# Kernel tuning notes

Hardware: AMD Instinct MI355X
Metric: run time of the kernel (lower is better)

Reference implementation:

```python
import jax, jax.numpy as jnp
import numpy as np

B, NI, NO = 32, 64, 64


def setup_inputs() -> dict:
    key = jax.random.key(0)
    k1, k2, k3, k4, k5, k6 = jax.random.split(key, 6)
    return {
        "input_re": jax.random.normal(k1, (B, NI, NI), dtype=jnp.float32),
        "input_im": jax.random.normal(k2, (B, NI, NI), dtype=jnp.float32),
        "w_re": jax.random.normal(k3, (NI, NI, NO, NO), dtype=jnp.float32),
        "w_im": jax.random.normal(k4, (NI, NI, NO, NO), dtype=jnp.float32),
        "amp_weights": jax.random.normal(k5, (NI, NI), dtype=jnp.float32),
        "phase_weights": jax.random.normal(k6, (NI, NI), dtype=jnp.float32),
    }


def reference(input_re, input_im, w_re, w_im, amp_weights, phase_weights):
    # complex input field (B, NI, NI) and diffraction kernel (NI, NI, NO, NO)
    e_in = jax.lax.complex(input_re, input_im)
    w_ip = jax.lax.complex(w_re, w_im)
    # passive transmission coefficients: sigmoid(amp) * exp(i*phase)
    ts = (jax.nn.sigmoid(amp_weights)
          * jnp.exp(1j * phase_weights.astype(jnp.complex64))).astype(jnp.complex64)
    # modulated field, then sum over input pixels (i,j) -> complex GEMM
    modulated = e_in * ts[None, :, :]                    # (B, NI, NI)
    out = jnp.einsum('bij,ijkl->bkl', modulated, w_ip)   # (B, NO, NO)
    return out
```

## Files before the change

kernel.cpp:

```cpp
#include <hip/hip_runtime.h>
#include <cstdint>
#include <cstddef>

#define KC 4096
#define NN 4096
#define NB 32
#define HALF (NB * NN)

typedef __attribute__((ext_vector_type(8))) short  bf16x8;
typedef __attribute__((ext_vector_type(16))) float f32x16;

__device__ __forceinline__ unsigned short f2bf(float f) {
    union { float f; unsigned u; } v; v.f = f;
    unsigned r = v.u + 0x7fffu + ((v.u >> 16) & 1u);
    return (unsigned short)(r >> 16);
}

__global__ __launch_bounds__(256) void prep_kernel(
    const float* __restrict__ in_re, const float* __restrict__ in_im,
    const float* __restrict__ amp,   const float* __restrict__ phase,
    uint32_t* __restrict__ wsA)
{
    int tid = blockIdx.x * 256 + threadIdx.x;
    int b = tid >> 12;
    int k = tid & (KC - 1);
    float er = in_re[tid], ei = in_im[tid];
    float a = amp[k], p = phase[k];
    float s = 1.0f / (1.0f + expf(-a));
    float sn, cs;
    sincosf(p, &sn, &cs);
    float tr = s * cs, ti = s * sn;
    float mr = er * tr - ei * ti;
    float mi = er * ti + ei * tr;
    uint32_t pk = (uint32_t)f2bf(mr) | ((uint32_t)f2bf(mi) << 16);
    wsA[((((k >> 2) << 5) + b) << 2) | (k & 3)] = pk;
}

__global__ __launch_bounds__(256) void gemm_kernel(
    const float* __restrict__ w_re, const float* __restrict__ w_im,
    const bf16x8* __restrict__ wsA, float2* __restrict__ wsP, int steps)
{
    const int lane = threadIdx.x & 63;
    const int wave = threadIdx.x >> 6;
    const int h    = lane >> 5;
    const int l32  = lane & 31;
    const int n    = blockIdx.x * 128 + wave * 32 + l32;
    const int s    = blockIdx.y;
    const int kbase = s * (steps * 8);

    f32x16 accR = {};
    f32x16 accI = {};

    const bf16x8* aptr = wsA + ((size_t)(kbase >> 2) + h) * 32 + l32;
    const float* pre = w_re + (size_t)(kbase + h * 4) * NN + n;
    const float* pim = w_im + (size_t)(kbase + h * 4) * NN + n;

#pragma unroll 4
    for (int t = 0; t < steps; ++t) {
        bf16x8 afrag = aptr[(size_t)(2 * t) * 32];
        const float* pr = pre + (size_t)t * 8 * NN;
        const float* pi = pim + (size_t)t * 8 * NN;
        float r0 = pr[0], r1 = pr[NN], r2 = pr[2 * NN], r3 = pr[3 * NN];
        float i0 = pi[0], i1 = pi[NN], i2 = pi[2 * NN], i3 = pi[3 * NN];

        bf16x8 bR, bI;
        bR[0] = (short)f2bf(r0);  bR[1] = (short)f2bf(-i0);
        bR[2] = (short)f2bf(r1);  bR[3] = (short)f2bf(-i1);
        bR[4] = (short)f2bf(r2);  bR[5] = (short)f2bf(-i2);
        bR[6] = (short)f2bf(r3);  bR[7] = (short)f2bf(-i3);
        bI[0] = (short)f2bf(i0);  bI[1] = (short)f2bf(r0);
        bI[2] = (short)f2bf(i1);  bI[3] = (short)f2bf(r1);
        bI[4] = (short)f2bf(i2);  bI[5] = (short)f2bf(r2);
        bI[6] = (short)f2bf(i3);  bI[7] = (short)f2bf(r3);

        accR = __builtin_amdgcn_mfma_f32_32x32x16_bf16(afrag, bR, accR, 0, 0, 0);
        accI = __builtin_amdgcn_mfma_f32_32x32x16_bf16(afrag, bI, accI, 0, 0, 0);
    }

#pragma unroll
    for (int r = 0; r < 16; ++r) {
        int brow = (r & 3) + 8 * (r >> 2) + 4 * h;
        float2 v; v.x = accR[r]; v.y = accI[r];
        wsP[((size_t)s * NB + brow) * NN + n] = v;
    }
}

__global__ __launch_bounds__(256) void reduce_kernel(
    const float2* __restrict__ wsP, float* __restrict__ out, int S)
{
    int tid = blockIdx.x * 256 + threadIdx.x;
    float re = 0.f, im = 0.f;
    for (int s = 0; s < S; ++s) {
        float2 v = wsP[(size_t)s * (NB * NN) + tid];
        re += v.x; im += v.y;
    }
    out[tid]        = re;
    out[HALF + tid] = im;
}

extern "C" void kernel_launch(void* const* d_in, const int* in_sizes, int n_in,
                              void* d_out, int out_size, void* d_ws, size_t ws_size,
                              hipStream_t stream)
{
    const float* in_re  = (const float*)d_in[0];
    const float* in_im  = (const float*)d_in[1];
    const float* w_re   = (const float*)d_in[2];
    const float* w_im   = (const float*)d_in[3];
    const float* amp    = (const float*)d_in[4];
    const float* phase  = (const float*)d_in[5];

    const size_t A_BYTES = (size_t)1024 * 32 * 16;
    uint32_t* wsA = (uint32_t*)d_ws;
    float2*   wsP = (float2*)((char*)d_ws + A_BYTES);

    int S = 16;
    while (S > 1 && A_BYTES + (size_t)S * NB * NN * sizeof(float2) > ws_size) S >>= 1;
    int steps = (KC / S) / 8;

    prep_kernel<<<dim3((NB * KC) / 256), dim3(256), 0, stream>>>(
        in_re, in_im, amp, phase, wsA);

    gemm_kernel<<<dim3(NN / 128, S), dim3(256), 0, stream>>>(
        w_re, w_im, (const bf16x8*)wsA, wsP, steps);

    reduce_kernel<<<dim3((NB * NN) / 256), dim3(256), 0, stream>>>(
        wsP, (float*)d_out, S);
}
```

Measured before the change: 171.6 us.

## Stage GEMM operands through double-buffered LDS with async global-to-LDS loads

```diff
diff --git a/kernel.cpp b/kernel.cpp
--- a/kernel.cpp
+++ b/kernel.cpp
@@ -26,9 +26,9 @@
     int k = tid & (KC - 1);
     float er = in_re[tid], ei = in_im[tid];
     float a = amp[k], p = phase[k];
-    float s = 1.0f / (1.0f + expf(-a));
-    float sn, cs;
-    sincosf(p, &sn, &cs);
+    float s = 1.0f / (1.0f + __expf(-a));
+    float sn = __sinf(p);
+    float cs = __cosf(p);
     float tr = s * cs, ti = s * sn;
     float mr = er * tr - ei * ti;
     float mi = er * ti + ei * tr;
@@ -36,32 +36,52 @@
     wsA[((((k >> 2) << 5) + b) << 2) | (k & 3)] = pk;
 }
 
-__global__ __launch_bounds__(256) void gemm_kernel(
+__global__ __launch_bounds__(256, 4) void gemm_kernel(
     const float* __restrict__ w_re, const float* __restrict__ w_im,
-    const bf16x8* __restrict__ wsA, float2* __restrict__ wsP, int steps)
+    const uint32_t* __restrict__ wsA, float2* __restrict__ wsP, int steps)
 {
-    const int lane = threadIdx.x & 63;
-    const int wave = threadIdx.x >> 6;
+    __shared__ float    ldsW[2][2][8][128];
+    __shared__ uint32_t ldsA[2][256];
+
+    const int tid  = threadIdx.x;
+    const int lane = tid & 63;
+    const int wave = tid >> 6;
     const int h    = lane >> 5;
     const int l32  = lane & 31;
     const int n    = blockIdx.x * 128 + wave * 32 + l32;
     const int s    = blockIdx.y;
     const int kbase = s * (steps * 8);
 
+    const int row8 = tid >> 5;
+    const int nof  = (tid & 31) << 2;
+    const float* gre = w_re + (size_t)(kbase + row8) * NN + blockIdx.x * 128 + nof;
+    const float* gim = w_im + (size_t)(kbase + row8) * NN + blockIdx.x * 128 + nof;
+    const uint32_t* ga = wsA + (size_t)(kbase >> 2) * 128 + tid;
+
     f32x16 accR = {};
     f32x16 accI = {};
 
-    const bf16x8* aptr = wsA + ((size_t)(kbase >> 2) + h) * 32 + l32;
-    const float* pre = w_re + (size_t)(kbase + h * 4) * NN + n;
-    const float* pim = w_im + (size_t)(kbase + h * 4) * NN + n;
+    auto STAGE = [&](int t, int bb) {
+        __builtin_amdgcn_global_load_lds(
+            (const __attribute__((address_space(1))) void*)(gre + (size_t)t * 8 * NN),
+            (__attribute__((address_space(3))) void*)(&ldsW[bb][0][2 * wave][0]),
+            16, 0, 0);
+        __builtin_amdgcn_global_load_lds(
+            (const __attribute__((address_space(1))) void*)(gim + (size_t)t * 8 * NN),
+            (__attribute__((address_space(3))) void*)(&ldsW[bb][1][2 * wave][0]),
+            16, 0, 0);
+        __builtin_amdgcn_global_load_lds(
+            (const __attribute__((address_space(1))) void*)(ga + (size_t)t * 256),
+            (__attribute__((address_space(3))) void*)(&ldsA[bb][wave * 64]),
+            4, 0, 0);
+    };
 
-#pragma unroll 4
-    for (int t = 0; t < steps; ++t) {
-        bf16x8 afrag = aptr[(size_t)(2 * t) * 32];
-        const float* pr = pre + (size_t)t * 8 * NN;
-        const float* pi = pim + (size_t)t * 8 * NN;
-        float r0 = pr[0], r1 = pr[NN], r2 = pr[2 * NN], r3 = pr[3 * NN];
-        float i0 = pi[0], i1 = pi[NN], i2 = pi[2 * NN], i3 = pi[3 * NN];
+    auto COMPUTE = [&](int bb) {
+        bf16x8 afrag = *(const bf16x8*)&ldsA[bb][h * 128 + l32 * 4];
+        const float* Lre = &ldsW[bb][0][h * 4][wave * 32 + l32];
+        const float* Lim = &ldsW[bb][1][h * 4][wave * 32 + l32];
+        float r0 = Lre[0], r1 = Lre[128], r2 = Lre[256], r3 = Lre[384];
+        float i0 = Lim[0], i1 = Lim[128], i2 = Lim[256], i3 = Lim[384];
 
         bf16x8 bR, bI;
         bR[0] = (short)f2bf(r0);  bR[1] = (short)f2bf(-i0);
@@ -75,7 +95,19 @@
 
         accR = __builtin_amdgcn_mfma_f32_32x32x16_bf16(afrag, bR, accR, 0, 0, 0);
         accI = __builtin_amdgcn_mfma_f32_32x32x16_bf16(afrag, bI, accI, 0, 0, 0);
+    };
+
+    STAGE(0, 0);
+    for (int t = 0; t < steps - 1; ++t) {
+        STAGE(t + 1, (t + 1) & 1);
+        asm volatile("s_waitcnt vmcnt(3)" ::: "memory");
+        __builtin_amdgcn_s_barrier();
+        COMPUTE(t & 1);
+        __builtin_amdgcn_s_barrier();
     }
+    asm volatile("s_waitcnt vmcnt(0)" ::: "memory");
+    __builtin_amdgcn_s_barrier();
+    COMPUTE((steps - 1) & 1);
 
 #pragma unroll
     for (int r = 0; r < 16; ++r) {
@@ -86,16 +118,19 @@
 }
 
 __global__ __launch_bounds__(256) void reduce_kernel(
-    const float2* __restrict__ wsP, float* __restrict__ out, int S)
+    const float4* __restrict__ wsP, float* __restrict__ out, int S)
 {
     int tid = blockIdx.x * 256 + threadIdx.x;
-    float re = 0.f, im = 0.f;
+    float re0 = 0.f, im0 = 0.f, re1 = 0.f, im1 = 0.f;
+#pragma unroll 8
     for (int s = 0; s < S; ++s) {
-        float2 v = wsP[(size_t)s * (NB * NN) + tid];
-        re += v.x; im += v.y;
+        float4 v = wsP[(size_t)s * (NB * NN / 2) + tid];
+        re0 += v.x; im0 += v.y; re1 += v.z; im1 += v.w;
     }
-    out[tid]        = re;
-    out[HALF + tid] = im;
+    float2* o_re = (float2*)out + tid;
+    float2* o_im = (float2*)(out + HALF) + tid;
+    *o_re = make_float2(re0, re1);
+    *o_im = make_float2(im0, im1);
 }
 
 extern "C" void kernel_launch(void* const* d_in, const int* in_sizes, int n_in,
@@ -113,7 +148,7 @@
     uint32_t* wsA = (uint32_t*)d_ws;
     float2*   wsP = (float2*)((char*)d_ws + A_BYTES);
 
-    int S = 16;
+    int S = 32;
     while (S > 1 && A_BYTES + (size_t)S * NB * NN * sizeof(float2) > ws_size) S >>= 1;
     int steps = (KC / S) / 8;
 
@@ -121,8 +156,8 @@
         in_re, in_im, amp, phase, wsA);
 
     gemm_kernel<<<dim3(NN / 128, S), dim3(256), 0, stream>>>(
-        w_re, w_im, (const bf16x8*)wsA, wsP, steps);
+        w_re, w_im, wsA, wsP, steps);
 
-    reduce_kernel<<<dim3((NB * NN) / 256), dim3(256), 0, stream>>>(
-        wsP, (float*)d_out, S);
+    reduce_kernel<<<dim3((NB * NN / 2) / 256), dim3(256), 0, stream>>>(
+        (const float4*)wsP, (float*)d_out, S);
 }
```

After: 170.8 us. No clear change (-0.5%).
